# Kernel optimization log

Hardware: AMD Instinct MI355X
Metric: run time of the kernel (lower is better)

The kernel has to match this reference:

```python
import jax, jax.numpy as jnp
import numpy as np

N = 50000
E = 1600000
IN_C = 64
HID = 16
HEADS = 4
OUT_C = 1
ATT_SLOPE = 0.2   # GATConv negative_slope for attention logits
ACT_SLOPE = 0.01  # F.leaky_relu default between layers


def _glorot(key, shape):
    fan_in, fan_out = shape[0], shape[-1]
    lim = jnp.sqrt(6.0 / (fan_in + fan_out))
    return jax.random.uniform(key, shape, jnp.float32, -lim, lim)


def setup_inputs() -> dict:
    key = jax.random.key(0)
    ks = jax.random.split(key, 12)
    x = jax.random.normal(ks[0], (N, IN_C), jnp.float32)
    edge_index = jax.random.randint(ks[1], (2, E), 0, N, jnp.int64)
    return {
        "x": x,
        "edge_index": edge_index,
        # GAT layer 1: in -> HID per head, HEADS heads (concat)
        "W1": _glorot(ks[2], (IN_C, HEADS * HID)),
        "att_src1": _glorot(ks[3], (HEADS, HID)),
        "att_dst1": _glorot(ks[4], (HEADS, HID)),
        "b1": jnp.zeros((HEADS * HID,), jnp.float32),
        # GAT layer 2: HEADS*HID -> HID, 1 head
        "W2": _glorot(ks[5], (HEADS * HID, HID)),
        "att_src2": _glorot(ks[6], (1, HID)),
        "att_dst2": _glorot(ks[7], (1, HID)),
        "b2": jnp.zeros((HID,), jnp.float32),
        # final linear
        "Wo": _glorot(ks[8], (HID, OUT_C)),
        "bo": jnp.zeros((OUT_C,), jnp.float32),
    }


def _gat_layer(x, src, dst, W, a_src, a_dst, b, n_nodes):
    """PyG GATConv (eval mode): h = xW; edge logits from additive attention;
    segment softmax over incoming edges of each dst; weighted scatter-sum."""
    H, C = a_src.shape
    h = (x @ W).reshape(n_nodes, H, C)                       # [N, H, C]
    alpha_s = jnp.einsum("nhc,hc->nh", h, a_src)             # [N, H]
    alpha_d = jnp.einsum("nhc,hc->nh", h, a_dst)             # [N, H]
    e = jax.nn.leaky_relu(alpha_s[src] + alpha_d[dst], ATT_SLOPE)  # [E, H]
    m = jax.ops.segment_max(e, dst, num_segments=n_nodes)    # [N, H]
    w = jnp.exp(e - m[dst])
    denom = jax.ops.segment_sum(w, dst, num_segments=n_nodes)
    alpha = w / denom[dst]                                   # [E, H] (self-loops => denom>0)
    out = jax.ops.segment_sum(h[src] * alpha[:, :, None], dst, num_segments=n_nodes)
    return out.reshape(n_nodes, H * C) + b                   # concat heads + bias


def reference(x, edge_index, W1, att_src1, att_dst1, b1,
              W2, att_src2, att_dst2, b2, Wo, bo):
    n = x.shape[0]
    loops = jnp.arange(n, dtype=edge_index.dtype)
    src = jnp.concatenate([edge_index[0], loops])            # add_self_loops=True
    dst = jnp.concatenate([edge_index[1], loops])
    h = _gat_layer(x, src, dst, W1, att_src1, att_dst1, b1, n)
    h = jax.nn.leaky_relu(h, ACT_SLOPE)
    h = _gat_layer(h, src, dst, W2, att_src2, att_dst2, b2, n)
    h = jax.nn.leaky_relu(h, ACT_SLOPE)
    return h @ Wo + bo                                       # [N, 1]
```

## Files before the change

### kernel.cpp

```cpp
#include <hip/hip_runtime.h>
#include <hip/hip_bf16.h>
#include <cstdint>

#define N_NODES 50000
#define N_EDGES 1600000
#define EE (N_EDGES + N_NODES)
#define BSH 7
#define BSIZE 128
#define NBUCKET ((N_NODES + BSIZE - 1) >> BSH)
#define CSH 13
#define CAP 8192
#define BIN_BLOCKS 403
#define GEMM_BLOCKS 3125

__device__ __forceinline__ float lrelu(float x, float s) { return x >= 0.f ? x : s * x; }
__device__ __forceinline__ float bflo(uint32_t v) { return __uint_as_float(v << 16); }
__device__ __forceinline__ float bfhi(uint32_t v) { return __uint_as_float(v & 0xFFFF0000u); }
__device__ __forceinline__ uint32_t packbf(float a, float b) {
    uint32_t ua = __float_as_uint(a), ub = __float_as_uint(b);
    ua += 0x7FFF + ((ua >> 16) & 1);
    ub += 0x7FFF + ((ub >> 16) & 1);
    return (ua >> 16) | (ub & 0xFFFF0000u);
}
__device__ __forceinline__ float rdlane(float v, int l) {
    return __uint_as_float(__builtin_amdgcn_readlane(__float_as_uint(v), l));
}

__global__ __launch_bounds__(256) void k_pre(
    const float* __restrict__ x, const float* __restrict__ W1,
    const float* __restrict__ as_w, const float* __restrict__ ad_w,
    uint32_t* __restrict__ h1b, float* __restrict__ as1, float* __restrict__ ad1,
    const int* __restrict__ src, const int* __restrict__ dst,
    int* __restrict__ bcur, uint32_t* __restrict__ binned) {
    if (blockIdx.x < BIN_BLOCKS) {
        __shared__ int lcnt[NBUCKET];
        __shared__ int lbase[NBUCKET];
        const int T = 16;
        for (int i = threadIdx.x; i < NBUCKET; i += 256) lcnt[i] = 0;
        __syncthreads();
        uint32_t pv[T];
        uint32_t pm[T];
        int base = blockIdx.x * (256 * T);
        if (base + 256 * T <= N_EDGES) {
            const int4* s4 = (const int4*)(src + base);
            const int4* d4 = (const int4*)(dst + base);
#pragma unroll
            for (int k = 0; k < 4; k++) {
                int4 sv = s4[threadIdx.x + k * 256];
                int4 dv = d4[threadIdx.x + k * 256];
                int ss[4] = {sv.x, sv.y, sv.z, sv.w};
                int dd[4] = {dv.x, dv.y, dv.z, dv.w};
#pragma unroll
                for (int j = 0; j < 4; j++) {
                    int b = dd[j] >> BSH;
                    int r = atomicAdd(&lcnt[b], 1);
                    pv[k * 4 + j] = (uint32_t)ss[j] | ((uint32_t)(dd[j] & (BSIZE - 1)) << 16);
                    pm[k * 4 + j] = (uint32_t)r | ((uint32_t)b << 16);
                }
            }
        } else {
#pragma unroll
            for (int k = 0; k < T; k++) {
                int e = base + ((k & 3) * 4 + (k >> 2)) * 256 + threadIdx.x;
                pm[k] = 0xFFFFFFFFu;
                if (e < EE) {
                    int s, d;
                    if (e < N_EDGES) { s = src[e]; d = dst[e]; } else { s = e - N_EDGES; d = s; }
                    int b = d >> BSH;
                    int r = atomicAdd(&lcnt[b], 1);
                    pv[k] = (uint32_t)s | ((uint32_t)(d & (BSIZE - 1)) << 16);
                    pm[k] = (uint32_t)r | ((uint32_t)b << 16);
                }
            }
        }
        __syncthreads();
        for (int i = threadIdx.x; i < NBUCKET; i += 256) {
            int c = lcnt[i];
            if (c) lbase[i] = atomicAdd(&bcur[i], c);
        }
        __syncthreads();
#pragma unroll
        for (int k = 0; k < T; k++) {
            if (pm[k] != 0xFFFFFFFFu) {
                int b = pm[k] >> 16, r = pm[k] & 0xFFFF;
                binned[((size_t)b << CSH) + lbase[b] + r] = pv[k];
            }
        }
        return;
    }
    int c = threadIdx.x & 63;
    int wv = threadIdx.x >> 6;
    float wreg[64];
#pragma unroll
    for (int k = 0; k < 64; k++) wreg[k] = W1[k * 64 + c];
    float aw = as_w[c];
    float dw = ad_w[c];
    int base = (blockIdx.x - BIN_BLOCKS) * 16 + wv * 4;
#pragma unroll
    for (int r = 0; r < 4; r++) {
        int n = base + r;
        float xr = x[n * 64 + c];
        float a0 = 0.f, a1 = 0.f, a2 = 0.f, a3 = 0.f;
#pragma unroll
        for (int k = 0; k < 64; k += 4) {
            a0 = fmaf(rdlane(xr, k),     wreg[k],     a0);
            a1 = fmaf(rdlane(xr, k + 1), wreg[k + 1], a1);
            a2 = fmaf(rdlane(xr, k + 2), wreg[k + 2], a2);
            a3 = fmaf(rdlane(xr, k + 3), wreg[k + 3], a3);
        }
        float acc = (a0 + a1) + (a2 + a3);
        float other = __shfl_xor(acc, 1, 64);
        if (!(c & 1)) h1b[n * 32 + (c >> 1)] = packbf(acc, other);
        float asv = acc * aw;
        float adv = acc * dw;
#pragma unroll
        for (int off = 1; off < 16; off <<= 1) {
            asv += __shfl_xor(asv, off, 64);
            adv += __shfl_xor(adv, off, 64);
        }
        if ((c & 15) == 0) { as1[n * 4 + (c >> 4)] = asv; ad1[n * 4 + (c >> 4)] = adv; }
    }
}

__global__ __launch_bounds__(1024) void kB_sort_aggr1(
    const int* __restrict__ bcur, const uint32_t* __restrict__ binned,
    int* __restrict__ rowdesc, unsigned short* __restrict__ esrc,
    const float* __restrict__ as1, const float* __restrict__ ad1,
    const uint32_t* __restrict__ h1b,
    const float* __restrict__ b1, const float* __restrict__ W2,
    const float* __restrict__ as2w, const float* __restrict__ ad2w,
    float* __restrict__ h2, float* __restrict__ as2, float* __restrict__ ad2) {
    int b = blockIdx.x, tid = threadIdx.x, wv = tid >> 6;
    int p0 = b << CSH;
    int L = bcur[b];
    __shared__ int cnt16[16][BSIZE];
    __shared__ int wbase[16][BSIZE];
    __shared__ int shs[BSIZE];
    __shared__ int sdesc[BSIZE];
    __shared__ unsigned short sesrc[CAP];
    for (int i = tid; i < 16 * BSIZE; i += 1024) ((int*)cnt16)[i] = 0;
    __syncthreads();

    uint32_t pv[8];
    unsigned short rk[8];
#pragma unroll
    for (int k = 0; k < 8; k++) {
        int i = tid + k * 1024;
        if (i < L) {
            uint32_t v = binned[p0 + i];
            pv[k] = v;
            rk[k] = (unsigned short)atomicAdd(&cnt16[wv][(v >> 16) & (BSIZE - 1)], 1);
        }
    }
    __syncthreads();

    int tot = 0;
    if (tid < BSIZE) {
#pragma unroll
        for (int w = 0; w < 16; w++) tot += cnt16[w][tid];
        shs[tid] = tot;
    }
    __syncthreads();
    for (int off = 1; off < BSIZE; off <<= 1) {
        int t = 0;
        if (tid < BSIZE && tid >= off) t = shs[tid - off];
        __syncthreads();
        if (tid < BSIZE && tid >= off) shs[tid] += t;
        __syncthreads();
    }
    if (tid < BSIZE) {
        int excl = shs[tid] - tot;
        int node = (b << BSH) + tid;
        int d = excl | (tot << 13);
        sdesc[tid] = d;
        if (node < N_NODES) rowdesc[node] = d;
        int wb = excl;
#pragma unroll
        for (int w = 0; w < 16; w++) { wbase[w][tid] = wb; wb += cnt16[w][tid]; }
    }
    __syncthreads();

#pragma unroll
    for (int k = 0; k < 8; k++) {
        int i = tid + k * 1024;
        if (i < L) {
            uint32_t v = pv[k];
            int dl = (v >> 16) & (BSIZE - 1);
            sesrc[wbase[wv][dl] + (int)rk[k]] = (unsigned short)(v & 0xFFFF);
        }
    }
    __syncthreads();

    for (int i = tid; i < L; i += 1024) esrc[p0 + i] = sesrc[i];

    int lane = tid & 63;
    int slot = lane >> 3, cl = lane & 7;
    int hc = cl >> 1;
    const uint4* h1b4 = (const uint4*)h1b;
    float4 bb0 = *(const float4*)(b1 + 8 * cl);
    float4 bb1 = *(const float4*)(b1 + 8 * cl + 4);
    int co = lane & 15, kg = lane >> 4;
    int l0 = 2 * kg, l1 = 2 * kg + 1;
    const float* w2r = W2 + (16 * kg) * 16 + co;
    float asw = as2w[co], adw = ad2w[co];

    for (int nn = 0; nn < 8; nn++) {
        int ln = (wv << 3) + nn;
        int n = (b << BSH) + ln;
        if (n >= N_NODES) break;
        int md = sdesc[ln];
        int begin = md & (CAP - 1);
        int deg = md >> 13;
        float ad1h = ad1[n * 4 + hc];

        float a0 = 0.f, a1 = 0.f, a2 = 0.f, a3 = 0.f, a4 = 0.f, a5 = 0.f, a6 = 0.f, a7 = 0.f, dsum = 0.f;
        int iters = (deg + 7) >> 3;
#pragma unroll 4
        for (int it = 0; it < iters; it++) {
            int idx = it * 8 + slot;
            int s = sesrc[begin + idx];
            float e = as1[s * 4 + hc] + ad1h;
            float w = __expf(e >= 0.f ? e : 0.2f * e);
            w = (idx < deg) ? w : 0.f;
            uint4 v = h1b4[s * 8 + cl];
            dsum += w;
            a0 += w * bflo(v.x); a1 += w * bfhi(v.x);
            a2 += w * bflo(v.y); a3 += w * bfhi(v.y);
            a4 += w * bflo(v.z); a5 += w * bfhi(v.z);
            a6 += w * bflo(v.w); a7 += w * bfhi(v.w);
        }
#pragma unroll
        for (int off = 8; off <= 32; off <<= 1) {
            a0 += __shfl_xor(a0, off, 64); a1 += __shfl_xor(a1, off, 64);
            a2 += __shfl_xor(a2, off, 64); a3 += __shfl_xor(a3, off, 64);
            a4 += __shfl_xor(a4, off, 64); a5 += __shfl_xor(a5, off, 64);
            a6 += __shfl_xor(a6, off, 64); a7 += __shfl_xor(a7, off, 64);
            dsum += __shfl_xor(dsum, off, 64);
        }
        float dinv = 1.f / dsum;

        float act0 = lrelu(a0 * dinv + bb0.x, 0.01f);
        float act1 = lrelu(a1 * dinv + bb0.y, 0.01f);
        float act2 = lrelu(a2 * dinv + bb0.z, 0.01f);
        float act3 = lrelu(a3 * dinv + bb0.w, 0.01f);
        float act4 = lrelu(a4 * dinv + bb1.x, 0.01f);
        float act5 = lrelu(a5 * dinv + bb1.y, 0.01f);
        float act6 = lrelu(a6 * dinv + bb1.z, 0.01f);
        float act7 = lrelu(a7 * dinv + bb1.w, 0.01f);

        float g = 0.f;
        g = fmaf(__shfl(act0, l0, 64), w2r[0 * 16],  g);
        g = fmaf(__shfl(act1, l0, 64), w2r[1 * 16],  g);
        g = fmaf(__shfl(act2, l0, 64), w2r[2 * 16],  g);
        g = fmaf(__shfl(act3, l0, 64), w2r[3 * 16],  g);
        g = fmaf(__shfl(act4, l0, 64), w2r[4 * 16],  g);
        g = fmaf(__shfl(act5, l0, 64), w2r[5 * 16],  g);
        g = fmaf(__shfl(act6, l0, 64), w2r[6 * 16],  g);
        g = fmaf(__shfl(act7, l0, 64), w2r[7 * 16],  g);
        g = fmaf(__shfl(act0, l1, 64), w2r[8 * 16],  g);
        g = fmaf(__shfl(act1, l1, 64), w2r[9 * 16],  g);
        g = fmaf(__shfl(act2, l1, 64), w2r[10 * 16], g);
        g = fmaf(__shfl(act3, l1, 64), w2r[11 * 16], g);
        g = fmaf(__shfl(act4, l1, 64), w2r[12 * 16], g);
        g = fmaf(__shfl(act5, l1, 64), w2r[13 * 16], g);
        g = fmaf(__shfl(act6, l1, 64), w2r[14 * 16], g);
        g = fmaf(__shfl(act7, l1, 64), w2r[15 * 16], g);
        g += __shfl_xor(g, 16, 64);
        g += __shfl_xor(g, 32, 64);
        if (lane < 16) h2[n * 16 + co] = g;
        float asv = g * asw;
        float adv2 = g * adw;
#pragma unroll
        for (int off = 1; off < 16; off <<= 1) {
            asv += __shfl_xor(asv, off, 64);
            adv2 += __shfl_xor(adv2, off, 64);
        }
        if (lane == 0) { as2[n] = asv; ad2[n] = adv2; }
    }
}

__global__ __launch_bounds__(256) void k_aggr2(
    const int* __restrict__ rowdesc, const unsigned short* __restrict__ esrc,
    const float* __restrict__ as2, const float* __restrict__ ad2,
    const float* __restrict__ h2,
    const float* __restrict__ b2, const float* __restrict__ Wo,
    const float* __restrict__ bo, float* __restrict__ out) {
    int n = blockIdx.x * 4 + (threadIdx.x >> 6);
    int lane = threadIdx.x & 63;
    int md = rowdesc[n];
    int begin = ((n >> BSH) << CSH) + (md & (CAP - 1));
    int deg = md >> 13;
    float adv = ad2[n];

    int slot = lane >> 3, c2 = lane & 7;
    const float2* h22 = (const float2*)h2;
    float acc0 = 0.f, acc1 = 0.f, dsum = 0.f;

    int iters = (deg + 7) >> 3;
#pragma unroll 4
    for (int it = 0; it < iters; it++) {
        int idx = it * 8 + slot;
        int s = esrc[begin + idx];
        float e = as2[s] + adv;
        float w = __expf(e >= 0.f ? e : 0.2f * e);
        w = (idx < deg) ? w : 0.f;
        float2 hv = h22[s * 8 + c2];
        acc0 += w * hv.x;
        acc1 += w * hv.y;
        dsum += w;
    }
#pragma unroll
    for (int off = 8; off <= 32; off <<= 1) {
        acc0 += __shfl_xor(acc0, off, 64);
        acc1 += __shfl_xor(acc1, off, 64);
        dsum += __shfl_xor(dsum, off, 64);
    }
    float v0 = lrelu(acc0 / dsum + b2[2 * c2], 0.01f) * Wo[2 * c2];
    float v1 = lrelu(acc1 / dsum + b2[2 * c2 + 1], 0.01f) * Wo[2 * c2 + 1];
    float y = v0 + v1;
    y += __shfl_xor(y, 1, 64);
    y += __shfl_xor(y, 2, 64);
    y += __shfl_xor(y, 4, 64);
    if (lane == 0) out[n] = y + bo[0];
}

extern "C" void kernel_launch(void* const* d_in, const int* in_sizes, int n_in,
                              void* d_out, int out_size, void* d_ws, size_t ws_size,
                              hipStream_t stream) {
    const float* x    = (const float*)d_in[0];
    const int*   ei   = (const int*)d_in[1];
    const float* W1   = (const float*)d_in[2];
    const float* as1w = (const float*)d_in[3];
    const float* ad1w = (const float*)d_in[4];
    const float* b1   = (const float*)d_in[5];
    const float* W2   = (const float*)d_in[6];
    const float* as2w = (const float*)d_in[7];
    const float* ad2w = (const float*)d_in[8];
    const float* b2   = (const float*)d_in[9];
    const float* Wo   = (const float*)d_in[10];
    const float* bo   = (const float*)d_in[11];
    float* out = (float*)d_out;

    const int* srcp = ei;
    const int* dstp = ei + N_EDGES;

    char* p = (char*)d_ws;
    auto alloc = [&](size_t bytes) -> char* {
        char* r = p;
        p += (bytes + 255) / 256 * 256;
        return r;
    };
    int*            bcur    = (int*)alloc((size_t)(NBUCKET + 1) * 4);
    int*            rowdesc = (int*)alloc((size_t)N_NODES * 4);
    uint32_t*       binned  = (uint32_t*)alloc((size_t)NBUCKET * CAP * 4);
    unsigned short* esrc    = (unsigned short*)alloc((size_t)NBUCKET * CAP * 2 + 256);
    float*          h2      = (float*)alloc((size_t)N_NODES * 16 * 4);
    uint32_t*       h1b     = (uint32_t*)alloc((size_t)N_NODES * 32 * 4);
    float*          as1     = (float*)alloc((size_t)N_NODES * 4 * 4);
    float*          ad1     = (float*)alloc((size_t)N_NODES * 4 * 4);
    float*          as2     = (float*)alloc((size_t)N_NODES * 4);
    float*          ad2     = (float*)alloc((size_t)N_NODES * 4);
    (void)alloc(4 * 1024 * 1024);

    hipMemsetAsync(bcur, 0, (size_t)(NBUCKET + 1) * 4, stream);

    k_pre<<<BIN_BLOCKS + GEMM_BLOCKS, 256, 0, stream>>>(x, W1, as1w, ad1w, h1b, as1, ad1,
                                                        srcp, dstp, bcur, binned);
    kB_sort_aggr1<<<NBUCKET, 1024, 0, stream>>>(bcur, binned, rowdesc, esrc,
                                                as1, ad1, h1b, b1, W2, as2w, ad2w, h2, as2, ad2);
    k_aggr2<<<N_NODES / 4, 256, 0, stream>>>(rowdesc, esrc, as2, ad2, h2, b2, Wo, bo, out);
}
```

Measured before the change: 199.3 us.

## Shrink sort buckets to 32 nodes with 256-thread blocks and shuffle scan

Reduces the destination bucket size from 128 to 32 nodes and the per-bucket capacity from 8192 to 2048 edges. The sort-and-aggregate kernel now runs with 256-thread blocks instead of 1024, which gives about four times as many blocks to spread over the GPU and a smaller shared-memory footprint. The multi-barrier shared-memory prefix scan is replaced by a single-wave shuffle scan. Neighbor index loads beyond the degree are now guarded so padded slots read node 0 rather than stale entries. The risk is overflow if any 32-node bucket receives more than 2048 edges, and each block now has fewer waves to hide gather latency.

```diff
diff --git a/kernel.cpp b/kernel.cpp
--- a/kernel.cpp
+++ b/kernel.cpp
@@ -5,11 +5,11 @@
 #define N_NODES 50000
 #define N_EDGES 1600000
 #define EE (N_EDGES + N_NODES)
-#define BSH 7
-#define BSIZE 128
+#define BSH 5
+#define BSIZE 32
 #define NBUCKET ((N_NODES + BSIZE - 1) >> BSH)
-#define CSH 13
-#define CAP 8192
+#define CSH 11
+#define CAP 2048
 #define BIN_BLOCKS 403
 #define GEMM_BLOCKS 3125
 
@@ -122,7 +122,7 @@
     }
 }
 
-__global__ __launch_bounds__(1024) void kB_sort_aggr1(
+__global__ __launch_bounds__(256) void kB_sort_aggr1(
     const int* __restrict__ bcur, const uint32_t* __restrict__ binned,
     int* __restrict__ rowdesc, unsigned short* __restrict__ esrc,
     const float* __restrict__ as1, const float* __restrict__ ad1,
@@ -133,56 +133,48 @@
     int b = blockIdx.x, tid = threadIdx.x, wv = tid >> 6;
     int p0 = b << CSH;
     int L = bcur[b];
-    __shared__ int cnt16[16][BSIZE];
-    __shared__ int wbase[16][BSIZE];
-    __shared__ int shs[BSIZE];
+    __shared__ int cnt4[4][BSIZE];
+    __shared__ int wbase[4][BSIZE];
     __shared__ int sdesc[BSIZE];
-    __shared__ unsigned short sesrc[CAP];
-    for (int i = tid; i < 16 * BSIZE; i += 1024) ((int*)cnt16)[i] = 0;
+    __shared__ unsigned short sesrc[CAP + 16];
+    for (int i = tid; i < 4 * BSIZE; i += 256) ((int*)cnt4)[i] = 0;
     __syncthreads();
 
     uint32_t pv[8];
     unsigned short rk[8];
 #pragma unroll
     for (int k = 0; k < 8; k++) {
-        int i = tid + k * 1024;
+        int i = tid + k * 256;
         if (i < L) {
             uint32_t v = binned[p0 + i];
             pv[k] = v;
-            rk[k] = (unsigned short)atomicAdd(&cnt16[wv][(v >> 16) & (BSIZE - 1)], 1);
+            rk[k] = (unsigned short)atomicAdd(&cnt4[wv][(v >> 16) & (BSIZE - 1)], 1);
         }
     }
     __syncthreads();
 
-    int tot = 0;
     if (tid < BSIZE) {
-#pragma unroll
-        for (int w = 0; w < 16; w++) tot += cnt16[w][tid];
-        shs[tid] = tot;
-    }
-    __syncthreads();
-    for (int off = 1; off < BSIZE; off <<= 1) {
-        int t = 0;
-        if (tid < BSIZE && tid >= off) t = shs[tid - off];
-        __syncthreads();
-        if (tid < BSIZE && tid >= off) shs[tid] += t;
-        __syncthreads();
-    }
-    if (tid < BSIZE) {
-        int excl = shs[tid] - tot;
+        int tot = cnt4[0][tid] + cnt4[1][tid] + cnt4[2][tid] + cnt4[3][tid];
+        int incl = tot;
+#pragma unroll
+        for (int off = 1; off < BSIZE; off <<= 1) {
+            int t = __shfl_up(incl, off, BSIZE);
+            if ((tid & (BSIZE - 1)) >= off) incl += t;
+        }
+        int excl = incl - tot;
         int node = (b << BSH) + tid;
         int d = excl | (tot << 13);
         sdesc[tid] = d;
         if (node < N_NODES) rowdesc[node] = d;
         int wb = excl;
 #pragma unroll
-        for (int w = 0; w < 16; w++) { wbase[w][tid] = wb; wb += cnt16[w][tid]; }
+        for (int w = 0; w < 4; w++) { wbase[w][tid] = wb; wb += cnt4[w][tid]; }
     }
     __syncthreads();
 
 #pragma unroll
     for (int k = 0; k < 8; k++) {
-        int i = tid + k * 1024;
+        int i = tid + k * 256;
         if (i < L) {
             uint32_t v = pv[k];
             int dl = (v >> 16) & (BSIZE - 1);
@@ -191,7 +183,7 @@
     }
     __syncthreads();
 
-    for (int i = tid; i < L; i += 1024) esrc[p0 + i] = sesrc[i];
+    for (int i = tid; i < L; i += 256) esrc[p0 + i] = sesrc[i];
 
     int lane = tid & 63;
     int slot = lane >> 3, cl = lane & 7;
@@ -218,10 +210,11 @@
 #pragma unroll 4
         for (int it = 0; it < iters; it++) {
             int idx = it * 8 + slot;
-            int s = sesrc[begin + idx];
+            bool ok = idx < deg;
+            int s = ok ? (int)sesrc[begin + idx] : 0;
             float e = as1[s * 4 + hc] + ad1h;
             float w = __expf(e >= 0.f ? e : 0.2f * e);
-            w = (idx < deg) ? w : 0.f;
+            w = ok ? w : 0.f;
             uint4 v = h1b4[s * 8 + cl];
             dsum += w;
             a0 += w * bflo(v.x); a1 += w * bfhi(v.x);
@@ -300,10 +293,11 @@
 #pragma unroll 4
     for (int it = 0; it < iters; it++) {
         int idx = it * 8 + slot;
-        int s = esrc[begin + idx];
+        bool ok = idx < deg;
+        int s = ok ? (int)esrc[begin + idx] : 0;
         float e = as2[s] + adv;
         float w = __expf(e >= 0.f ? e : 0.2f * e);
-        w = (idx < deg) ? w : 0.f;
+        w = ok ? w : 0.f;
         float2 hv = h22[s * 8 + c2];
         acc0 += w * hv.x;
         acc1 += w * hv.y;
@@ -366,7 +360,7 @@
 
     k_pre<<<BIN_BLOCKS + GEMM_BLOCKS, 256, 0, stream>>>(x, W1, as1w, ad1w, h1b, as1, ad1,
                                                         srcp, dstp, bcur, binned);
-    kB_sort_aggr1<<<NBUCKET, 1024, 0, stream>>>(bcur, binned, rowdesc, esrc,
-                                                as1, ad1, h1b, b1, W2, as2w, ad2w, h2, as2, ad2);
+    kB_sort_aggr1<<<NBUCKET, 256, 0, stream>>>(bcur, binned, rowdesc, esrc,
+                                               as1, ad1, h1b, b1, W2, as2w, ad2w, h2, as2, ad2);
     k_aggr2<<<N_NODES / 4, 256, 0, stream>>>(rowdesc, esrc, as2, ad2, h2, b2, Wo, bo, out);
 }
```

Result: faster. 193.7 us (-2.8%).
